# Kernel tuning notes

Measured on AMD Instinct MI355X. Metric: run time of the kernel, lower is better.

## Reference

```python
import jax, jax.numpy as jnp
import numpy as np

B, C, D, O = 64, 64, 512, 256
N_REG, G = 8, 8  # 8 regions of 8 channels


def setup_inputs() -> dict:
    key = jax.random.key(0)
    ks = jax.random.split(key, 9)
    std = 0.02  # init_weights_classify: normal(0, 0.02) for Linear weights, zero bias
    x = jax.random.normal(ks[0], (B, C, D), dtype=jnp.float32)
    region_indices = jnp.arange(C, dtype=jnp.int32).reshape(N_REG, G)
    # attn_fc: Linear(2D -> D), ReLU, Linear(D -> 1)
    W1 = jax.random.normal(ks[1], (2 * D, D), dtype=jnp.float32) * std
    b1 = jnp.zeros((D,), jnp.float32)
    W2 = jax.random.normal(ks[2], (D, 1), dtype=jnp.float32) * std
    b2 = jnp.zeros((1,), jnp.float32)
    # gcn1: Linear(D -> D); gcn2: Linear(D -> O)
    Wg1 = jax.random.normal(ks[3], (D, D), dtype=jnp.float32) * std
    bg1 = jnp.zeros((D,), jnp.float32)
    Wg2 = jax.random.normal(ks[4], (D, O), dtype=jnp.float32) * std
    bg2 = jnp.zeros((O,), jnp.float32)
    return {"x": x, "W1": W1, "b1": b1, "W2": W2, "b2": b2,
            "Wg1": Wg1, "bg1": bg1, "Wg2": Wg2, "bg2": bg2,
            "region_indices": region_indices}


def _leaky_relu02(z):
    return jnp.where(z >= 0, z, 0.2 * z)


def reference(x, W1, b1, W2, b2, Wg1, bg1, Wg2, bg2, region_indices):
    Bb, Cc, Dd = x.shape
    n_reg, g = region_indices.shape
    # channel -> region id; mask[i,j] = same region and i != j
    rid = jnp.zeros((Cc,), jnp.int32).at[region_indices.reshape(-1)].set(
        jnp.repeat(jnp.arange(n_reg, dtype=jnp.int32), g))
    idx = jnp.arange(Cc)
    mask = (rid[:, None] == rid[None, :]) & (idx[:, None] != idx[None, :])  # [C, C]
    # attn_fc on cat(x_i, x_j): split first linear to avoid [B,C,C,2D] concat
    a = x @ W1[:Dd]   # [B, C, D]
    bpart = x @ W1[Dd:]  # [B, C, D]
    h = jax.nn.relu(a[:, :, None, :] + bpart[:, None, :, :] + b1)  # [B, C, C, D]
    scores = jnp.einsum('bijd,do->bij', h, W2) + b2[0]  # [B, C, C]
    scores = jnp.where(mask[None, :, :], scores, -jnp.inf)
    adj = jax.nn.softmax(scores, axis=-1)  # [B, C, C]
    # gcn1: adj @ x -> Linear -> LeakyReLU(0.2); residual mix
    m1 = jnp.einsum('bij,bjd->bid', adj, x)
    x1 = _leaky_relu02(m1 @ Wg1 + bg1)
    x1 = 0.5 * x1 + 0.5 * x
    # gcn2
    m2 = jnp.einsum('bij,bjd->bid', adj, x1)
    out = _leaky_relu02(m2 @ Wg2 + bg2)  # [B, C, O]
    return out
```

## Files before the change

### kernel.cpp

```cpp
#include <hip/hip_runtime.h>
#include <math.h>

#define B_   64
#define C_   64
#define D_   512
#define O_   256
#define G_   8
#define M_   4096

typedef __attribute__((ext_vector_type(8))) short s16x8;
typedef __attribute__((ext_vector_type(4))) float f32x4;
typedef unsigned short u16;
typedef unsigned int   u32;

__device__ __forceinline__ float bf2f(u16 u) { return __uint_as_float(((u32)u) << 16); }
__device__ __forceinline__ u16 f2bf(float f) {
    u32 u = __float_as_uint(f);
    return (u16)((u + 0x7FFFu + ((u >> 16) & 1u)) >> 16);
}
__device__ __forceinline__ void gload16(const void* g, void* l) {
    __builtin_amdgcn_global_load_lds((const __attribute__((address_space(1))) u32*)g,
                                     (__attribute__((address_space(3))) u32*)l, 16, 0, 0);
}
__device__ __forceinline__ void xcd_swz(int& bx, int& by) {
    int nx = (int)gridDim.x;
    int L = bx + by * nx;
    int nwg = nx * (int)gridDim.y;
    int nid = (L & 7) * (nwg >> 3) + (L >> 3);
    bx = nid & (nx - 1);
    by = nid / nx;
}

__global__ __launch_bounds__(256)
void prep_kernel(const float* __restrict__ x, u16* __restrict__ x_bf,
                 const float* __restrict__ W1, u16* __restrict__ W1t,
                 const float* __restrict__ Wg1, u16* __restrict__ Wg1t,
                 const float* __restrict__ Wg2, u16* __restrict__ Wg2t)
{
    __shared__ float tile[32][33];
    const int bx = blockIdx.x, tid = threadIdx.x;
    if (bx < 1024) {
        size_t i = ((size_t)bx * 256 + tid) * 8;
        const float4* p = (const float4*)(x + i);
        float4 v0 = p[0], v1 = p[1];
        s16x8 o;
        o[0] = (short)f2bf(v0.x); o[1] = (short)f2bf(v0.y);
        o[2] = (short)f2bf(v0.z); o[3] = (short)f2bf(v0.w);
        o[4] = (short)f2bf(v1.x); o[5] = (short)f2bf(v1.y);
        o[6] = (short)f2bf(v1.z); o[7] = (short)f2bf(v1.w);
        *(s16x8*)(x_bf + i) = o;
        return;
    }
    const float* src; u16* dst; int k0, n0, nsrc, obase;
    if (bx < 1536) {
        int idx = bx - 1024, h = idx >> 8, t = idx & 255;
        src = W1 + (size_t)h * 512 * 512; dst = W1t; obase = h * 512;
        k0 = (t >> 4) * 32; n0 = (t & 15) * 32; nsrc = 512;
    } else if (bx < 1792) {
        int t = bx - 1536;
        src = Wg1; dst = Wg1t; obase = 0;
        k0 = (t >> 4) * 32; n0 = (t & 15) * 32; nsrc = 512;
    } else {
        int t = bx - 1792;
        src = Wg2; dst = Wg2t; obase = 0;
        k0 = (t >> 3) * 32; n0 = (t & 7) * 32; nsrc = 256;
    }
    int tx = tid & 31, ty = tid >> 5;
    #pragma unroll
    for (int j = 0; j < 4; j++)
        tile[ty + j * 8][tx] = src[(size_t)(k0 + ty + j * 8) * nsrc + n0 + tx];
    __syncthreads();
    #pragma unroll
    for (int j = 0; j < 4; j++)
        dst[(size_t)(obase + n0 + ty + j * 8) * 512 + k0 + tx] = f2bf(tile[tx][ty + j * 8]);
}

__global__ __launch_bounds__(512)
void gemm1_kernel(const u16* __restrict__ A, const u16* __restrict__ Bt,
                  u16* __restrict__ Obf0, u16* __restrict__ Obf1)
{
    constexpr int K = 512, BK = 64, NT = K / BK;
    __shared__ __align__(16) u16 As[2][128 * 64];
    __shared__ __align__(16) u16 Bs[2][128 * 64];

    const int tid = threadIdx.x;
    const int lane = tid & 63;
    const int w = tid >> 6;
    const int wr = w >> 1, wc = w & 1;
    const int lr = lane & 15, lq = lane >> 4;
    int bx = blockIdx.x, by = blockIdx.y;
    xcd_swz(bx, by);
    const int m0 = by * 128, n0 = bx * 128;

    const int sr = tid >> 3;
    const int ss = tid & 7;
    const int gsl = ss ^ (sr & 7);

    f32x4 acc[2][4] = {};

    auto stage = [&](int buf, int kt) {
        #pragma unroll
        for (int ch = 0; ch < 2; ch++)
            gload16(A + (size_t)(m0 + ch * 64 + sr) * K + kt + gsl * 8,
                    &As[buf][ch * 4096 + tid * 8]);
        #pragma unroll
        for (int ch = 0; ch < 2; ch++)
            gload16(Bt + (size_t)(n0 + ch * 64 + sr) * K + kt + gsl * 8,
                    &Bs[buf][ch * 4096 + tid * 8]);
    };

    stage(0, 0);
    int cur = 0;
    for (int t = 0; t < NT; t++) {
        __syncthreads();
        if (t + 1 < NT) stage(cur ^ 1, (t + 1) * BK);
        const u16* as = As[cur]; const u16* bs = Bs[cur];
        #pragma unroll
        for (int ks = 0; ks < 2; ks++) {
            s16x8 af[2], bfv[4];
            #pragma unroll
            for (int m = 0; m < 2; m++) {
                int r = wr * 32 + m * 16 + lr;
                af[m] = *(const s16x8*)(as + r * 64 + (((ks * 4 + lq) ^ (r & 7)) * 8));
            }
            #pragma unroll
            for (int n = 0; n < 4; n++) {
                int r = wc * 64 + n * 16 + lr;
                bfv[n] = *(const s16x8*)(bs + r * 64 + (((ks * 4 + lq) ^ (r & 7)) * 8));
            }
            #pragma unroll
            for (int m = 0; m < 2; m++)
                #pragma unroll
                for (int n = 0; n < 4; n++)
                    acc[m][n] = __builtin_amdgcn_mfma_f32_16x16x32_bf16(af[m], bfv[n], acc[m][n], 0, 0, 0);
        }
        cur ^= 1;
    }

    #pragma unroll
    for (int m = 0; m < 2; m++) {
        #pragma unroll
        for (int n = 0; n < 4; n++) {
            #pragma unroll
            for (int j = 0; j < 4; j++) {
                int row = m0 + wr * 32 + m * 16 + lq * 4 + j;
                int col = n0 + wc * 64 + n * 16 + lr;
                float v = acc[m][n][j];
                if (col < 512) Obf0[(size_t)row * 512 + col] = f2bf(v);
                else           Obf1[(size_t)row * 512 + col - 512] = f2bf(v);
            }
        }
    }
}

__global__ __launch_bounds__(256)
void scores_m1_kernel(const u16* __restrict__ a_bf, const u16* __restrict__ bp_bf,
                      const u16* __restrict__ x_bf,
                      const float* __restrict__ b1, const float* __restrict__ W2,
                      const float* __restrict__ b2,
                      const int* __restrict__ region_indices,
                      float* __restrict__ adjw, u16* __restrict__ m1)
{
    __shared__ __align__(16) u16 bp_lds[64 * 512];
    __shared__ int ri_lds[64];
    __shared__ int rid_lds[64];

    int L = blockIdx.x;
    int nid = ((L & 7) << 5) + (L >> 3);
    const int b = nid >> 2, q = nid & 3;
    const int tid = threadIdx.x, lane = tid & 63, w = tid >> 6;

    #pragma unroll
    for (int it = 0; it < 16; it++)
        gload16(bp_bf + (size_t)b * 32768 + it * 2048 + tid * 8, bp_lds + it * 2048 + tid * 8);
    if (tid < 64) {
        int c = region_indices[tid];
        ri_lds[tid] = c;
        rid_lds[c] = tid >> 3;
    }

    const int d0 = lane * 8;
    float4 b1a = *(const float4*)(b1 + d0), b1b = *(const float4*)(b1 + d0 + 4);
    float4 w2a = *(const float4*)(W2 + d0), w2b = *(const float4*)(W2 + d0 + 4);
    float b1v[8] = { b1a.x, b1a.y, b1a.z, b1a.w, b1b.x, b1b.y, b1b.z, b1b.w };
    float w2v[8] = { w2a.x, w2a.y, w2a.z, w2a.w, w2b.x, w2b.y, w2b.z, w2b.w };
    const float bias2 = b2[0];

    __syncthreads();

    for (int rr = 0; rr < 4; rr++) {
        const int i = q * 16 + w * 4 + rr;
        const int bi = b * 64 + i;
        const int r = rid_lds[i];
        int mem[8];
        #pragma unroll
        for (int m = 0; m < 8; m++) mem[m] = ri_lds[r * 8 + m];

        s16x8 a8 = *(const s16x8*)(a_bf + (size_t)bi * 512 + d0);
        float ai[8];
        #pragma unroll
        for (int t = 0; t < 8; t++) ai[t] = bf2f((u16)a8[t]) + b1v[t];

        float p[8];
        #pragma unroll
        for (int m = 0; m < 8; m++) {
            s16x8 bv = *(const s16x8*)(bp_lds + mem[m] * 512 + d0);
            float s = 0.f;
            #pragma unroll
            for (int t = 0; t < 8; t++) {
                float h = ai[t] + bf2f((u16)bv[t]);
                s += fmaxf(h, 0.f) * w2v[t];
            }
            p[m] = s;
        }
        #pragma unroll
        for (int off = 32; off >= 1; off >>= 1)
            #pragma unroll
            for (int m = 0; m < 8; m++) p[m] += __shfl_xor(p[m], off);

        float scmax = -INFINITY;
        #pragma unroll
        for (int m = 0; m < 8; m++) {
            p[m] = (mem[m] == i) ? -INFINITY : p[m] + bias2;
            scmax = fmaxf(scmax, p[m]);
        }
        float esum = 0.f;
        #pragma unroll
        for (int m = 0; m < 8; m++) {
            p[m] = (mem[m] == i) ? 0.f : __expf(p[m] - scmax);
            esum += p[m];
        }
        const float inv = 1.f / esum;

        float accv[8] = {};
        #pragma unroll
        for (int m = 0; m < 8; m++) {
            p[m] *= inv;
            s16x8 xv = *(const s16x8*)(x_bf + ((size_t)(b * 64 + mem[m])) * 512 + d0);
            #pragma unroll
            for (int t = 0; t < 8; t++) accv[t] += p[m] * bf2f((u16)xv[t]);
        }
        s16x8 o;
        #pragma unroll
        for (int t = 0; t < 8; t++) o[t] = (short)f2bf(accv[t]);
        *(s16x8*)(m1 + (size_t)bi * 512 + d0) = o;
        if (lane < 8) adjw[(size_t)bi * 8 + lane] = p[lane];
    }
}

__global__ __launch_bounds__(512)
void gemm2_m2_kernel(const u16* __restrict__ A, const u16* __restrict__ Bt,
                     const float* __restrict__ bias, const float* __restrict__ xres,
                     const float* __restrict__ adjw, const int* __restrict__ region_indices,
                     u16* __restrict__ m2)
{
    constexpr int K = 512, BK = 64, NT = K / BK;
    __shared__ __align__(16) u16 As[2][64 * 64];
    __shared__ __align__(16) u16 Bs[2][128 * 64];
    __shared__ __align__(16) u16 x1s[64 * 136];
    __shared__ int ri_lds[64];
    __shared__ int rid_lds[64];

    const int tid = threadIdx.x;
    const int lane = tid & 63;
    const int w = tid >> 6;
    const int wr = w >> 2, wc = w & 3;
    const int lr = lane & 15, lq = lane >> 4;
    int bx = blockIdx.x, by = blockIdx.y;
    xcd_swz(bx, by);
    const int b = by, n0 = bx * 128, m0 = b * 64;

    const int sr = tid >> 3, ss = tid & 7;
    const int gsl = ss ^ (sr & 7);

    if (tid < 64) {
        int c = region_indices[tid];
        ri_lds[tid] = c;
        rid_lds[c] = tid >> 3;
    }

    f32x4 acc[2][2] = {};

    auto stage = [&](int buf, int kt) {
        gload16(A + (size_t)(m0 + sr) * K + kt + gsl * 8, &As[buf][tid * 8]);
        #pragma unroll
        for (int ch = 0; ch < 2; ch++)
            gload16(Bt + (size_t)(n0 + ch * 64 + sr) * K + kt + gsl * 8,
                    &Bs[buf][ch * 4096 + tid * 8]);
    };

    stage(0, 0);
    int cur = 0;
    for (int t = 0; t < NT; t++) {
        __syncthreads();
        if (t + 1 < NT) stage(cur ^ 1, (t + 1) * BK);
        const u16* as = As[cur]; const u16* bs = Bs[cur];
        #pragma unroll
        for (int ks = 0; ks < 2; ks++) {
            s16x8 af[2], bfv[2];
            #pragma unroll
            for (int m = 0; m < 2; m++) {
                int r = wr * 32 + m * 16 + lr;
                af[m] = *(const s16x8*)(as + r * 64 + (((ks * 4 + lq) ^ (r & 7)) * 8));
            }
            #pragma unroll
            for (int n = 0; n < 2; n++) {
                int r = wc * 32 + n * 16 + lr;
                bfv[n] = *(const s16x8*)(bs + r * 64 + (((ks * 4 + lq) ^ (r & 7)) * 8));
            }
            #pragma unroll
            for (int m = 0; m < 2; m++)
                #pragma unroll
                for (int n = 0; n < 2; n++)
                    acc[m][n] = __builtin_amdgcn_mfma_f32_16x16x32_bf16(af[m], bfv[n], acc[m][n], 0, 0, 0);
        }
        cur ^= 1;
    }

    #pragma unroll
    for (int m = 0; m < 2; m++) {
        #pragma unroll
        for (int n = 0; n < 2; n++) {
            #pragma unroll
            for (int j = 0; j < 4; j++) {
                int lrow = wr * 32 + m * 16 + lq * 4 + j;
                int lcol = wc * 32 + n * 16 + lr;
                float v = acc[m][n][j] + bias[n0 + lcol];
                v = (v >= 0.f) ? v : 0.2f * v;
                v = 0.5f * v + 0.5f * xres[(size_t)(m0 + lrow) * 512 + n0 + lcol];
                x1s[lrow * 136 + lcol] = f2bf(v);
            }
        }
    }
    __syncthreads();

    const int i = tid >> 3, cb = tid & 7, c0 = cb * 16;
    const int bi = m0 + i;
    const int r = rid_lds[i];
    float acc2[16] = {};
    #pragma unroll
    for (int m = 0; m < 8; m++) {
        float wm = adjw[(size_t)bi * 8 + m];
        int j = ri_lds[r * 8 + m];
        #pragma unroll
        for (int cc = 0; cc < 2; cc++) {
            s16x8 v = *(const s16x8*)(x1s + j * 136 + c0 + cc * 8);
            #pragma unroll
            for (int t = 0; t < 8; t++) acc2[cc * 8 + t] += wm * bf2f((u16)v[t]);
        }
    }
    #pragma unroll
    for (int cc = 0; cc < 2; cc++) {
        s16x8 o;
        #pragma unroll
        for (int t = 0; t < 8; t++) o[t] = (short)f2bf(acc2[cc * 8 + t]);
        *(s16x8*)(m2 + (size_t)bi * 512 + n0 + c0 + cc * 8) = o;
    }
}

__global__ __launch_bounds__(256)
void gemm3_kernel(const u16* __restrict__ A, const u16* __restrict__ Bt,
                  const float* __restrict__ bias, float* __restrict__ Of)
{
    constexpr int K = 512, BK = 64, NT = K / BK;
    __shared__ __align__(16) u16 As[2][64 * 64];
    __shared__ __align__(16) u16 Bs[2][64 * 64];

    const int tid = threadIdx.x;
    const int lane = tid & 63;
    const int w = tid >> 6, wr = w >> 1, wc = w & 1;
    const int lr = lane & 15, lq = lane >> 4;
    int bx = blockIdx.x, by = blockIdx.y;
    xcd_swz(bx, by);
    const int m0 = by * 64, n0 = bx * 64;

    const int sr = tid >> 3, ss = tid & 7;
    const int gsl = ss ^ (sr & 7);

    f32x4 acc[2][2] = {};

    auto stage = [&](int buf, int kt) {
        #pragma unroll
        for (int ch = 0; ch < 2; ch++)
            gload16(A + (size_t)(m0 + ch * 32 + sr) * K + kt + gsl * 8,
                    &As[buf][ch * 2048 + tid * 8]);
        #pragma unroll
        for (int ch = 0; ch < 2; ch++)
            gload16(Bt + (size_t)(n0 + ch * 32 + sr) * K + kt + gsl * 8,
                    &Bs[buf][ch * 2048 + tid * 8]);
    };

    stage(0, 0);
    int cur = 0;
    for (int t = 0; t < NT; t++) {
        __syncthreads();
        if (t + 1 < NT) stage(cur ^ 1, (t + 1) * BK);
        const u16* as = As[cur]; const u16* bs = Bs[cur];
        #pragma unroll
        for (int ks = 0; ks < 2; ks++) {
            s16x8 af[2], bfv[2];
            #pragma unroll
            for (int m = 0; m < 2; m++) {
                int r = wr * 32 + m * 16 + lr;
                af[m] = *(const s16x8*)(as + r * 64 + (((ks * 4 + lq) ^ (r & 7)) * 8));
            }
            #pragma unroll
            for (int n = 0; n < 2; n++) {
                int r = wc * 32 + n * 16 + lr;
                bfv[n] = *(const s16x8*)(bs + r * 64 + (((ks * 4 + lq) ^ (r & 7)) * 8));
            }
            #pragma unroll
            for (int m = 0; m < 2; m++)
                #pragma unroll
                for (int n = 0; n < 2; n++)
                    acc[m][n] = __builtin_amdgcn_mfma_f32_16x16x32_bf16(af[m], bfv[n], acc[m][n], 0, 0, 0);
        }
        cur ^= 1;
    }

    #pragma unroll
    for (int m = 0; m < 2; m++) {
        #pragma unroll
        for (int n = 0; n < 2; n++) {
            #pragma unroll
            for (int j = 0; j < 4; j++) {
                int row = m0 + wr * 32 + m * 16 + lq * 4 + j;
                int col = n0 + wc * 32 + n * 16 + lr;
                float v = acc[m][n][j] + bias[col];
                v = (v >= 0.f) ? v : 0.2f * v;
                Of[(size_t)row * 256 + col] = v;
            }
        }
    }
}

extern "C" void kernel_launch(void* const* d_in, const int* in_sizes, int n_in,
                              void* d_out, int out_size, void* d_ws, size_t ws_size,
                              hipStream_t stream) {
    const float* x    = (const float*)d_in[0];
    const float* W1   = (const float*)d_in[1];
    const float* b1   = (const float*)d_in[2];
    const float* W2   = (const float*)d_in[3];
    const float* b2   = (const float*)d_in[4];
    const float* Wg1  = (const float*)d_in[5];
    const float* bg1  = (const float*)d_in[6];
    const float* Wg2  = (const float*)d_in[7];
    const float* bg2  = (const float*)d_in[8];
    const int* region_indices = (const int*)d_in[9];
    float* out = (float*)d_out;

    char* ws = (char*)d_ws;
    const size_t MB = 1024 * 1024;
    u16*   x_bf  = (u16*)(ws);
    u16*   W1t   = (u16*)(ws + 4 * MB);
    u16*   Wg1t  = (u16*)(ws + 5 * MB);
    u16*   Wg2t  = (u16*)(ws + 5 * MB + 512 * 1024);
    u16*   a_bf  = (u16*)(ws + 6 * MB);
    u16*   bp_bf = (u16*)(ws + 10 * MB);
    u16*   m1_bf = (u16*)(ws + 14 * MB);
    u16*   m2_bf = (u16*)(ws + 18 * MB);
    float* adjw  = (float*)(ws + 22 * MB);

    prep_kernel<<<1920, 256, 0, stream>>>(x, x_bf, W1, W1t, Wg1, Wg1t, Wg2, Wg2t);

    gemm1_kernel<<<dim3(8, 32), 512, 0, stream>>>(x_bf, W1t, a_bf, bp_bf);

    scores_m1_kernel<<<256, 256, 0, stream>>>(a_bf, bp_bf, x_bf, b1, W2, b2,
                                              region_indices, adjw, m1_bf);

    gemm2_m2_kernel<<<dim3(4, 64), 512, 0, stream>>>(
        m1_bf, Wg1t, bg1, x, adjw, region_indices, m2_bf);

    gemm3_kernel<<<dim3(4, 64), 256, 0, stream>>>(m2_bf, Wg2t, bg2, out);
}
```

Before: 119.2 us.

## Fuse five kernels into one persistent kernel with software grid barriers

Replaces the prep, gemm1, scores, gemm2 and gemm3 launches with a single persistent kernel of 256 workgroups of 512 threads, separated by atomic-counter grid barriers. The aim is to remove per-launch overhead and inter-kernel gaps for a small problem. Per-stage work is redistributed to fit the fixed 256-block grid, for example two rows per wave in the scores stage. In exchange it relies on all 256 blocks being co-resident, adds barrier spin cost, and needs a memset before each launch.

```diff
diff --git a/kernel.cpp b/kernel.cpp
--- a/kernel.cpp
+++ b/kernel.cpp
@@ -22,415 +22,361 @@
     __builtin_amdgcn_global_load_lds((const __attribute__((address_space(1))) u32*)g,
                                      (__attribute__((address_space(3))) u32*)l, 16, 0, 0);
 }
-__device__ __forceinline__ void xcd_swz(int& bx, int& by) {
-    int nx = (int)gridDim.x;
-    int L = bx + by * nx;
-    int nwg = nx * (int)gridDim.y;
-    int nid = (L & 7) * (nwg >> 3) + (L >> 3);
-    bx = nid & (nx - 1);
-    by = nid / nx;
+__device__ __forceinline__ int swz256(int L) { return (L & 7) * 32 + (L >> 3); }
+
+__device__ __forceinline__ void grid_barrier(u32* bar, int tid, int nb) {
+    __syncthreads();
+    if (tid == 0) {
+        __threadfence();
+        u32 gen = __hip_atomic_load(bar + 1, __ATOMIC_RELAXED, __HIP_MEMORY_SCOPE_AGENT);
+        u32 arrived = __hip_atomic_fetch_add(bar, 1u, __ATOMIC_ACQ_REL, __HIP_MEMORY_SCOPE_AGENT);
+        if (arrived == (u32)nb - 1) {
+            __hip_atomic_store(bar, 0u, __ATOMIC_RELAXED, __HIP_MEMORY_SCOPE_AGENT);
+            __hip_atomic_fetch_add(bar + 1, 1u, __ATOMIC_RELEASE, __HIP_MEMORY_SCOPE_AGENT);
+        } else {
+            while (__hip_atomic_load(bar + 1, __ATOMIC_ACQUIRE, __HIP_MEMORY_SCOPE_AGENT) == gen)
+                __builtin_amdgcn_s_sleep(8);
+        }
+        __threadfence();
+    }
+    __syncthreads();
 }
 
-__global__ __launch_bounds__(256)
-void prep_kernel(const float* __restrict__ x, u16* __restrict__ x_bf,
-                 const float* __restrict__ W1, u16* __restrict__ W1t,
-                 const float* __restrict__ Wg1, u16* __restrict__ Wg1t,
-                 const float* __restrict__ Wg2, u16* __restrict__ Wg2t)
+#define SMEM_BYTES 69632
+
+__global__ __launch_bounds__(512)
+void fused_kernel(const float* __restrict__ x, const float* __restrict__ W1,
+                  const float* __restrict__ b1, const float* __restrict__ W2,
+                  const float* __restrict__ b2, const float* __restrict__ Wg1,
+                  const float* __restrict__ bg1, const float* __restrict__ Wg2,
+                  const float* __restrict__ bg2, const int* __restrict__ region_indices,
+                  float* __restrict__ out,
+                  u16* __restrict__ x_bf, u16* __restrict__ W1t, u16* __restrict__ Wg1t,
+                  u16* __restrict__ Wg2t, u16* __restrict__ a_bf, u16* __restrict__ bp_bf,
+                  u16* __restrict__ m1_bf, u16* __restrict__ m2_bf,
+                  float* __restrict__ adjw, u32* __restrict__ bar)
 {
-    __shared__ float tile[32][33];
-    const int bx = blockIdx.x, tid = threadIdx.x;
-    if (bx < 1024) {
-        size_t i = ((size_t)bx * 256 + tid) * 8;
-        const float4* p = (const float4*)(x + i);
-        float4 v0 = p[0], v1 = p[1];
-        s16x8 o;
-        o[0] = (short)f2bf(v0.x); o[1] = (short)f2bf(v0.y);
-        o[2] = (short)f2bf(v0.z); o[3] = (short)f2bf(v0.w);
-        o[4] = (short)f2bf(v1.x); o[5] = (short)f2bf(v1.y);
-        o[6] = (short)f2bf(v1.z); o[7] = (short)f2bf(v1.w);
-        *(s16x8*)(x_bf + i) = o;
-        return;
-    }
-    const float* src; u16* dst; int k0, n0, nsrc, obase;
-    if (bx < 1536) {
-        int idx = bx - 1024, h = idx >> 8, t = idx & 255;
-        src = W1 + (size_t)h * 512 * 512; dst = W1t; obase = h * 512;
-        k0 = (t >> 4) * 32; n0 = (t & 15) * 32; nsrc = 512;
-    } else if (bx < 1792) {
-        int t = bx - 1536;
-        src = Wg1; dst = Wg1t; obase = 0;
-        k0 = (t >> 4) * 32; n0 = (t & 15) * 32; nsrc = 512;
-    } else {
-        int t = bx - 1792;
-        src = Wg2; dst = Wg2t; obase = 0;
-        k0 = (t >> 3) * 32; n0 = (t & 7) * 32; nsrc = 256;
-    }
-    int tx = tid & 31, ty = tid >> 5;
-    #pragma unroll
-    for (int j = 0; j < 4; j++)
-        tile[ty + j * 8][tx] = src[(size_t)(k0 + ty + j * 8) * nsrc + n0 + tx];
-    __syncthreads();
-    #pragma unroll
-    for (int j = 0; j < 4; j++)
-        dst[(size_t)(obase + n0 + ty + j * 8) * 512 + k0 + tx] = f2bf(tile[tx][ty + j * 8]);
-}
-
-__global__ __launch_bounds__(512)
-void gemm1_kernel(const u16* __restrict__ A, const u16* __restrict__ Bt,
-                  u16* __restrict__ Obf0, u16* __restrict__ Obf1)
-{
-    constexpr int K = 512, BK = 64, NT = K / BK;
-    __shared__ __align__(16) u16 As[2][128 * 64];
-    __shared__ __align__(16) u16 Bs[2][128 * 64];
-
-    const int tid = threadIdx.x;
-    const int lane = tid & 63;
-    const int w = tid >> 6;
-    const int wr = w >> 1, wc = w & 1;
+    __shared__ __align__(16) char sm[SMEM_BYTES];
+    const int wg = blockIdx.x, tid = threadIdx.x;
+    const int lane = tid & 63, w = tid >> 6;
     const int lr = lane & 15, lq = lane >> 4;
-    int bx = blockIdx.x, by = blockIdx.y;
-    xcd_swz(bx, by);
-    const int m0 = by * 128, n0 = bx * 128;
-
-    const int sr = tid >> 3;
-    const int ss = tid & 7;
-    const int gsl = ss ^ (sr & 7);
-
-    f32x4 acc[2][4] = {};
-
-    auto stage = [&](int buf, int kt) {
-        #pragma unroll
-        for (int ch = 0; ch < 2; ch++)
-            gload16(A + (size_t)(m0 + ch * 64 + sr) * K + kt + gsl * 8,
-                    &As[buf][ch * 4096 + tid * 8]);
-        #pragma unroll
-        for (int ch = 0; ch < 2; ch++)
-            gload16(Bt + (size_t)(n0 + ch * 64 + sr) * K + kt + gsl * 8,
-                    &Bs[buf][ch * 4096 + tid * 8]);
-    };
-
-    stage(0, 0);
-    int cur = 0;
-    for (int t = 0; t < NT; t++) {
+    const int sr = tid >> 3, ss = tid & 7, gsl = ss ^ (sr & 7);
+    const int NB = 256;
+
+    {
+        #pragma unroll
+        for (int s = 0; s < 2; s++) {
+            size_t i = ((size_t)(s * 256 + wg) * 512 + tid) * 8;
+            const float4* p = (const float4*)(x + i);
+            float4 v0 = p[0], v1 = p[1];
+            s16x8 o;
+            o[0]=(short)f2bf(v0.x); o[1]=(short)f2bf(v0.y); o[2]=(short)f2bf(v0.z); o[3]=(short)f2bf(v0.w);
+            o[4]=(short)f2bf(v1.x); o[5]=(short)f2bf(v1.y); o[6]=(short)f2bf(v1.z); o[7]=(short)f2bf(v1.w);
+            *(s16x8*)(x_bf + i) = o;
+        }
+        float (*tile)[32][33] = (float(*)[32][33])sm;
+        const int team = tid >> 8, t = tid & 255;
+        const int tx = t & 31, ty = t >> 5;
+        for (int u = 0; u < 2; u++) {
+            int tile_id = wg * 2 + team + 512 * u;
+            const float* src = nullptr; u16* dst = nullptr;
+            int k0 = 0, n0 = 0, nsrc = 0, obase = 0;
+            if (tile_id < 512) {
+                int h = tile_id >> 8, tt = tile_id & 255;
+                src = W1 + (size_t)h * 512 * 512; dst = W1t; obase = h * 512;
+                k0 = (tt >> 4) * 32; n0 = (tt & 15) * 32; nsrc = 512;
+            } else if (tile_id < 768) {
+                int tt = tile_id - 512; src = Wg1; dst = Wg1t;
+                k0 = (tt >> 4) * 32; n0 = (tt & 15) * 32; nsrc = 512;
+            } else if (tile_id < 896) {
+                int tt = tile_id - 768; src = Wg2; dst = Wg2t;
+                k0 = (tt >> 3) * 32; n0 = (tt & 7) * 32; nsrc = 256;
+            }
+            if (src) {
+                #pragma unroll
+                for (int j = 0; j < 4; j++)
+                    tile[team][ty + j * 8][tx] = src[(size_t)(k0 + ty + j * 8) * nsrc + n0 + tx];
+            }
+            __syncthreads();
+            if (src) {
+                #pragma unroll
+                for (int j = 0; j < 4; j++)
+                    dst[(size_t)(obase + n0 + ty + j * 8) * 512 + k0 + tx] =
+                        f2bf(tile[team][tx][ty + j * 8]);
+            }
+            __syncthreads();
+        }
+    }
+    grid_barrier(bar, tid, NB);
+
+    {
+        u16* As = (u16*)sm;
+        u16* Bs = (u16*)(sm + 32768);
+        const int nid = swz256(wg);
+        const int m0 = (nid >> 3) * 128, n0 = (nid & 7) * 128;
+        const int wr = w >> 1, wc = w & 1;
+        f32x4 acc[2][4] = {};
+        auto stage = [&](int buf, int kt) {
+            #pragma unroll
+            for (int ch = 0; ch < 2; ch++)
+                gload16(x_bf + (size_t)(m0 + ch * 64 + sr) * 512 + kt + gsl * 8,
+                        As + buf * 8192 + ch * 4096 + tid * 8);
+            #pragma unroll
+            for (int ch = 0; ch < 2; ch++)
+                gload16(W1t + (size_t)(n0 + ch * 64 + sr) * 512 + kt + gsl * 8,
+                        Bs + buf * 8192 + ch * 4096 + tid * 8);
+        };
+        stage(0, 0);
+        int cur = 0;
+        for (int t = 0; t < 8; t++) {
+            __syncthreads();
+            if (t < 7) stage(cur ^ 1, (t + 1) * 64);
+            const u16* as = As + cur * 8192;
+            const u16* bs = Bs + cur * 8192;
+            #pragma unroll
+            for (int ks = 0; ks < 2; ks++) {
+                s16x8 af[2], bfv[4];
+                #pragma unroll
+                for (int m = 0; m < 2; m++) {
+                    int r = wr * 32 + m * 16 + lr;
+                    af[m] = *(const s16x8*)(as + r * 64 + (((ks * 4 + lq) ^ (r & 7)) * 8));
+                }
+                #pragma unroll
+                for (int n = 0; n < 4; n++) {
+                    int r = wc * 64 + n * 16 + lr;
+                    bfv[n] = *(const s16x8*)(bs + r * 64 + (((ks * 4 + lq) ^ (r & 7)) * 8));
+                }
+                #pragma unroll
+                for (int m = 0; m < 2; m++)
+                    #pragma unroll
+                    for (int n = 0; n < 4; n++)
+                        acc[m][n] = __builtin_amdgcn_mfma_f32_16x16x32_bf16(af[m], bfv[n], acc[m][n], 0, 0, 0);
+            }
+            cur ^= 1;
+        }
+        #pragma unroll
+        for (int m = 0; m < 2; m++)
+            #pragma unroll
+            for (int n = 0; n < 4; n++)
+                #pragma unroll
+                for (int j = 0; j < 4; j++) {
+                    int row = m0 + wr * 32 + m * 16 + lq * 4 + j;
+                    int col = n0 + wc * 64 + n * 16 + lr;
+                    float v = acc[m][n][j];
+                    if (col < 512) a_bf[(size_t)row * 512 + col] = f2bf(v);
+                    else           bp_bf[(size_t)row * 512 + col - 512] = f2bf(v);
+                }
+    }
+    grid_barrier(bar, tid, NB);
+
+    {
+        u16* bp  = (u16*)sm;
+        int* ri  = (int*)(sm + 65536);
+        int* rid = (int*)(sm + 65536 + 256);
+        const int nid = swz256(wg);
+        const int b = nid >> 2, q = nid & 3;
+        #pragma unroll
+        for (int it = 0; it < 8; it++)
+            gload16(bp_bf + (size_t)b * 32768 + it * 4096 + tid * 8, bp + it * 4096 + tid * 8);
+        if (tid < 64) { int c = region_indices[tid]; ri[tid] = c; rid[c] = tid >> 3; }
+
+        const int d0 = lane * 8;
+        float4 b1a = *(const float4*)(b1 + d0), b1b = *(const float4*)(b1 + d0 + 4);
+        float4 w2a = *(const float4*)(W2 + d0), w2b = *(const float4*)(W2 + d0 + 4);
+        float b1v[8] = { b1a.x, b1a.y, b1a.z, b1a.w, b1b.x, b1b.y, b1b.z, b1b.w };
+        float w2v[8] = { w2a.x, w2a.y, w2a.z, w2a.w, w2b.x, w2b.y, w2b.z, w2b.w };
+        const float bias2 = b2[0];
         __syncthreads();
-        if (t + 1 < NT) stage(cur ^ 1, (t + 1) * BK);
-        const u16* as = As[cur]; const u16* bs = Bs[cur];
-        #pragma unroll
-        for (int ks = 0; ks < 2; ks++) {
-            s16x8 af[2], bfv[4];
-            #pragma unroll
-            for (int m = 0; m < 2; m++) {
-                int r = wr * 32 + m * 16 + lr;
-                af[m] = *(const s16x8*)(as + r * 64 + (((ks * 4 + lq) ^ (r & 7)) * 8));
-            }
-            #pragma unroll
-            for (int n = 0; n < 4; n++) {
-                int r = wc * 64 + n * 16 + lr;
-                bfv[n] = *(const s16x8*)(bs + r * 64 + (((ks * 4 + lq) ^ (r & 7)) * 8));
-            }
-            #pragma unroll
-            for (int m = 0; m < 2; m++)
-                #pragma unroll
-                for (int n = 0; n < 4; n++)
-                    acc[m][n] = __builtin_amdgcn_mfma_f32_16x16x32_bf16(af[m], bfv[n], acc[m][n], 0, 0, 0);
-        }
-        cur ^= 1;
-    }
-
-    #pragma unroll
-    for (int m = 0; m < 2; m++) {
-        #pragma unroll
-        for (int n = 0; n < 4; n++) {
+
+        #pragma unroll
+        for (int rr = 0; rr < 2; rr++) {
+            const int i = q * 16 + w * 2 + rr;
+            const int bi = b * 64 + i;
+            const int r = rid[i];
+            int mem[8];
+            #pragma unroll
+            for (int m = 0; m < 8; m++) mem[m] = ri[r * 8 + m];
+
+            s16x8 a8 = *(const s16x8*)(a_bf + (size_t)bi * 512 + d0);
+            float ai[8];
+            #pragma unroll
+            for (int t = 0; t < 8; t++) ai[t] = bf2f((u16)a8[t]) + b1v[t];
+
+            float p[8];
+            #pragma unroll
+            for (int m = 0; m < 8; m++) {
+                s16x8 bv = *(const s16x8*)(bp + mem[m] * 512 + d0);
+                float s = 0.f;
+                #pragma unroll
+                for (int t = 0; t < 8; t++) {
+                    float h = ai[t] + bf2f((u16)bv[t]);
+                    s += fmaxf(h, 0.f) * w2v[t];
+                }
+                p[m] = s;
+            }
+            #pragma unroll
+            for (int off = 32; off >= 1; off >>= 1)
+                #pragma unroll
+                for (int m = 0; m < 8; m++) p[m] += __shfl_xor(p[m], off);
+
+            float scmax = -INFINITY;
+            #pragma unroll
+            for (int m = 0; m < 8; m++) {
+                p[m] = (mem[m] == i) ? -INFINITY : p[m] + bias2;
+                scmax = fmaxf(scmax, p[m]);
+            }
+            float esum = 0.f;
+            #pragma unroll
+            for (int m = 0; m < 8; m++) {
+                p[m] = (mem[m] == i) ? 0.f : __expf(p[m] - scmax);
+                esum += p[m];
+            }
+            const float inv = 1.f / esum;
+
+            float accv[8] = {};
+            #pragma unroll
+            for (int m = 0; m < 8; m++) {
+                p[m] *= inv;
+                s16x8 xv = *(const s16x8*)(x_bf + ((size_t)(b * 64 + mem[m])) * 512 + d0);
+                #pragma unroll
+                for (int t = 0; t < 8; t++) accv[t] += p[m] * bf2f((u16)xv[t]);
+            }
+            s16x8 o;
+            #pragma unroll
+            for (int t = 0; t < 8; t++) o[t] = (short)f2bf(accv[t]);
+            *(s16x8*)(m1_bf + (size_t)bi * 512 + d0) = o;
+            if (lane < 8) adjw[(size_t)bi * 8 + lane] = p[lane];
+        }
+    }
+    grid_barrier(bar, tid, NB);
+
+    {
+        u16* As  = (u16*)sm;
+        u16* Bs  = (u16*)(sm + 16384);
+        u16* x1s = (u16*)(sm + 49152);
+        int* ri  = (int*)(sm + 66560);
+        int* rid = (int*)(sm + 66816);
+        const int nid = swz256(wg);
+        const int b = nid >> 2, n0 = (nid & 3) * 128, m0 = b * 64;
+        const int wr = w >> 2, wc = w & 3;
+        if (tid < 64) { int c = region_indices[tid]; ri[tid] = c; rid[c] = tid >> 3; }
+
+        f32x4 acc[2][2] = {};
+        auto stage = [&](int buf, int kt) {
+            gload16(m1_bf + (size_t)(m0 + sr) * 512 + kt + gsl * 8, As + buf * 4096 + tid * 8);
+            #pragma unroll
+            for (int ch = 0; ch < 2; ch++)
+                gload16(Wg1t + (size_t)(n0 + ch * 64 + sr) * 512 + kt + gsl * 8,
+                        Bs + buf * 8192 + ch * 4096 + tid * 8);
+        };
+        stage(0, 0);
+        int cur = 0;
+        for (int t = 0; t < 8; t++) {
+            __syncthreads();
+            if (t < 7) stage(cur ^ 1, (t + 1) * 64);
+            const u16* as = As + cur * 4096;
+            const u16* bs = Bs + cur * 8192;
+            #pragma unroll
+            for (int ks = 0; ks < 2; ks++) {
+                s16x8 af[2], bfv[2];
+                #pragma unroll
+                for (int m = 0; m < 2; m++) {
+                    int r = wr * 32 + m * 16 + lr;
+                    af[m] = *(const s16x8*)(as + r * 64 + (((ks * 4 + lq) ^ (r & 7)) * 8));
+                }
+                #pragma unroll
+                for (int n = 0; n < 2; n++) {
+                    int r = wc * 32 + n * 16 + lr;
+                    bfv[n] = *(const s16x8*)(bs + r * 64 + (((ks * 4 + lq) ^ (r & 7)) * 8));
+                }
+                #pragma unroll
+                for (int m = 0; m < 2; m++)
+                    #pragma unroll
+                    for (int n = 0; n < 2; n++)
+                        acc[m][n] = __builtin_amdgcn_mfma_f32_16x16x32_bf16(af[m], bfv[n], acc[m][n], 0, 0, 0);
+            }
+            cur ^= 1;
+        }
+        #pragma unroll
+        for (int m = 0; m < 2; m++)
+            #pragma unroll
+            for (int n = 0; n < 2; n++)
+                #pragma unroll
+                for (int j = 0; j < 4; j++) {
+                    int lrow = wr * 32 + m * 16 + lq * 4 + j;
+                    int lcol = wc * 32 + n * 16 + lr;
+                    float v = acc[m][n][j] + bg1[n0 + lcol];
+                    v = (v >= 0.f) ? v : 0.2f * v;
+                    v = 0.5f * v + 0.5f * x[(size_t)(m0 + lrow) * 512 + n0 + lcol];
+                    x1s[lrow * 136 + lcol] = f2bf(v);
+                }
+        __syncthreads();
+        const int i = tid >> 3, cb = tid & 7, c0 = cb * 16;
+        const int bi = m0 + i;
+        const int r = rid[i];
+        float acc2[16] = {};
+        #pragma unroll
+        for (int m = 0; m < 8; m++) {
+            float wm = adjw[(size_t)bi * 8 + m];
+            int j = ri[r * 8 + m];
+            #pragma unroll
+            for (int cc = 0; cc < 2; cc++) {
+                s16x8 v = *(const s16x8*)(x1s + j * 136 + c0 + cc * 8);
+                #pragma unroll
+                for (int t = 0; t < 8; t++) acc2[cc * 8 + t] += wm * bf2f((u16)v[t]);
+            }
+        }
+        #pragma unroll
+        for (int cc = 0; cc < 2; cc++) {
+            s16x8 o;
+            #pragma unroll
+            for (int t = 0; t < 8; t++) o[t] = (short)f2bf(acc2[cc * 8 + t]);
+            *(s16x8*)(m2_bf + (size_t)bi * 512 + n0 + c0 + cc * 8) = o;
+        }
+    }
+    grid_barrier(bar, tid, NB);
+
+    {
+        u16* As = (u16*)sm;
+        u16* Bs = (u16*)(sm + 16384);
+        const int nid = swz256(wg);
+        const int m0 = (nid >> 2) * 64, n0 = (nid & 3) * 64;
+        const int wr = w >> 1, wc = w & 1;
+        f32x4 acc[2] = {};
+        auto stage = [&](int buf, int kt) {
+            gload16(m2_bf + (size_t)(m0 + sr) * 512 + kt + gsl * 8, As + buf * 4096 + tid * 8);
+            gload16(Wg2t + (size_t)(n0 + sr) * 512 + kt + gsl * 8, Bs + buf * 4096 + tid * 8);
+        };
+        stage(0, 0);
+        int cur = 0;
+        for (int t = 0; t < 8; t++) {
+            __syncthreads();
+            if (t < 7) stage(cur ^ 1, (t + 1) * 64);
+            const u16* as = As + cur * 4096;
+            const u16* bs = Bs + cur * 4096;
+            #pragma unroll
+            for (int ks = 0; ks < 2; ks++) {
+                int ra = wr * 16 + lr;
+                s16x8 af = *(const s16x8*)(as + ra * 64 + (((ks * 4 + lq) ^ (ra & 7)) * 8));
+                #pragma unroll
+                for (int n = 0; n < 2; n++) {
+                    int r = wc * 32 + n * 16 + lr;
+                    s16x8 bv = *(const s16x8*)(bs + r * 64 + (((ks * 4 + lq) ^ (r & 7)) * 8));
+                    acc[n] = __builtin_amdgcn_mfma_f32_16x16x32_bf16(af, bv, acc[n], 0, 0, 0);
+                }
+            }
+            cur ^= 1;
+        }
+        #pragma unroll
+        for (int n = 0; n < 2; n++)
             #pragma unroll
             for (int j = 0; j < 4; j++) {
-                int row = m0 + wr * 32 + m * 16 + lq * 4 + j;
-                int col = n0 + wc * 64 + n * 16 + lr;
-                float v = acc[m][n][j];
-                if (col < 512) Obf0[(size_t)row * 512 + col] = f2bf(v);
-                else           Obf1[(size_t)row * 512 + col - 512] = f2bf(v);
-            }
-        }
-    }
-}
-
-__global__ __launch_bounds__(256)
-void scores_m1_kernel(const u16* __restrict__ a_bf, const u16* __restrict__ bp_bf,
-                      const u16* __restrict__ x_bf,
-                      const float* __restrict__ b1, const float* __restrict__ W2,
-                      const float* __restrict__ b2,
-                      const int* __restrict__ region_indices,
-                      float* __restrict__ adjw, u16* __restrict__ m1)
-{
-    __shared__ __align__(16) u16 bp_lds[64 * 512];
-    __shared__ int ri_lds[64];
-    __shared__ int rid_lds[64];
-
-    int L = blockIdx.x;
-    int nid = ((L & 7) << 5) + (L >> 3);
-    const int b = nid >> 2, q = nid & 3;
-    const int tid = threadIdx.x, lane = tid & 63, w = tid >> 6;
-
-    #pragma unroll
-    for (int it = 0; it < 16; it++)
-        gload16(bp_bf + (size_t)b * 32768 + it * 2048 + tid * 8, bp_lds + it * 2048 + tid * 8);
-    if (tid < 64) {
-        int c = region_indices[tid];
-        ri_lds[tid] = c;
-        rid_lds[c] = tid >> 3;
-    }
-
-    const int d0 = lane * 8;
-    float4 b1a = *(const float4*)(b1 + d0), b1b = *(const float4*)(b1 + d0 + 4);
-    float4 w2a = *(const float4*)(W2 + d0), w2b = *(const float4*)(W2 + d0 + 4);
-    float b1v[8] = { b1a.x, b1a.y, b1a.z, b1a.w, b1b.x, b1b.y, b1b.z, b1b.w };
-    float w2v[8] = { w2a.x, w2a.y, w2a.z, w2a.w, w2b.x, w2b.y, w2b.z, w2b.w };
-    const float bias2 = b2[0];
-
-    __syncthreads();
-
-    for (int rr = 0; rr < 4; rr++) {
-        const int i = q * 16 + w * 4 + rr;
-        const int bi = b * 64 + i;
-        const int r = rid_lds[i];
-        int mem[8];
-        #pragma unroll
-        for (int m = 0; m < 8; m++) mem[m] = ri_lds[r * 8 + m];
-
-        s16x8 a8 = *(const s16x8*)(a_bf + (size_t)bi * 512 + d0);
-        float ai[8];
-        #pragma unroll
-        for (int t = 0; t < 8; t++) ai[t] = bf2f((u16)a8[t]) + b1v[t];
-
-        float p[8];
-        #pragma unroll
-        for (int m = 0; m < 8; m++) {
-            s16x8 bv = *(const s16x8*)(bp_lds + mem[m] * 512 + d0);
-            float s = 0.f;
-            #pragma unroll
-            for (int t = 0; t < 8; t++) {
-                float h = ai[t] + bf2f((u16)bv[t]);
-                s += fmaxf(h, 0.f) * w2v[t];
-            }
-            p[m] = s;
-        }
-        #pragma unroll
-        for (int off = 32; off >= 1; off >>= 1)
-            #pragma unroll
-            for (int m = 0; m < 8; m++) p[m] += __shfl_xor(p[m], off);
-
-        float scmax = -INFINITY;
-        #pragma unroll
-        for (int m = 0; m < 8; m++) {
-            p[m] = (mem[m] == i) ? -INFINITY : p[m] + bias2;
-            scmax = fmaxf(scmax, p[m]);
-        }
-        float esum = 0.f;
-        #pragma unroll
-        for (int m = 0; m < 8; m++) {
-            p[m] = (mem[m] == i) ? 0.f : __expf(p[m] - scmax);
-            esum += p[m];
-        }
-        const float inv = 1.f / esum;
-
-        float accv[8] = {};
-        #pragma unroll
-        for (int m = 0; m < 8; m++) {
-            p[m] *= inv;
-            s16x8 xv = *(const s16x8*)(x_bf + ((size_t)(b * 64 + mem[m])) * 512 + d0);
-            #pragma unroll
-            for (int t = 0; t < 8; t++) accv[t] += p[m] * bf2f((u16)xv[t]);
-        }
-        s16x8 o;
-        #pragma unroll
-        for (int t = 0; t < 8; t++) o[t] = (short)f2bf(accv[t]);
-        *(s16x8*)(m1 + (size_t)bi * 512 + d0) = o;
-        if (lane < 8) adjw[(size_t)bi * 8 + lane] = p[lane];
-    }
-}
-
-__global__ __launch_bounds__(512)
-void gemm2_m2_kernel(const u16* __restrict__ A, const u16* __restrict__ Bt,
-                     const float* __restrict__ bias, const float* __restrict__ xres,
-                     const float* __restrict__ adjw, const int* __restrict__ region_indices,
-                     u16* __restrict__ m2)
-{
-    constexpr int K = 512, BK = 64, NT = K / BK;
-    __shared__ __align__(16) u16 As[2][64 * 64];
-    __shared__ __align__(16) u16 Bs[2][128 * 64];
-    __shared__ __align__(16) u16 x1s[64 * 136];
-    __shared__ int ri_lds[64];
-    __shared__ int rid_lds[64];
-
-    const int tid = threadIdx.x;
-    const int lane = tid & 63;
-    const int w = tid >> 6;
-    const int wr = w >> 2, wc = w & 3;
-    const int lr = lane & 15, lq = lane >> 4;
-    int bx = blockIdx.x, by = blockIdx.y;
-    xcd_swz(bx, by);
-    const int b = by, n0 = bx * 128, m0 = b * 64;
-
-    const int sr = tid >> 3, ss = tid & 7;
-    const int gsl = ss ^ (sr & 7);
-
-    if (tid < 64) {
-        int c = region_indices[tid];
-        ri_lds[tid] = c;
-        rid_lds[c] = tid >> 3;
-    }
-
-    f32x4 acc[2][2] = {};
-
-    auto stage = [&](int buf, int kt) {
-        gload16(A + (size_t)(m0 + sr) * K + kt + gsl * 8, &As[buf][tid * 8]);
-        #pragma unroll
-        for (int ch = 0; ch < 2; ch++)
-            gload16(Bt + (size_t)(n0 + ch * 64 + sr) * K + kt + gsl * 8,
-                    &Bs[buf][ch * 4096 + tid * 8]);
-    };
-
-    stage(0, 0);
-    int cur = 0;
-    for (int t = 0; t < NT; t++) {
-        __syncthreads();
-        if (t + 1 < NT) stage(cur ^ 1, (t + 1) * BK);
-        const u16* as = As[cur]; const u16* bs = Bs[cur];
-        #pragma unroll
-        for (int ks = 0; ks < 2; ks++) {
-            s16x8 af[2], bfv[2];
-            #pragma unroll
-            for (int m = 0; m < 2; m++) {
-                int r = wr * 32 + m * 16 + lr;
-                af[m] = *(const s16x8*)(as + r * 64 + (((ks * 4 + lq) ^ (r & 7)) * 8));
-            }
-            #pragma unroll
-            for (int n = 0; n < 2; n++) {
-                int r = wc * 32 + n * 16 + lr;
-                bfv[n] = *(const s16x8*)(bs + r * 64 + (((ks * 4 + lq) ^ (r & 7)) * 8));
-            }
-            #pragma unroll
-            for (int m = 0; m < 2; m++)
-                #pragma unroll
-                for (int n = 0; n < 2; n++)
-                    acc[m][n] = __builtin_amdgcn_mfma_f32_16x16x32_bf16(af[m], bfv[n], acc[m][n], 0, 0, 0);
-        }
-        cur ^= 1;
-    }
-
-    #pragma unroll
-    for (int m = 0; m < 2; m++) {
-        #pragma unroll
-        for (int n = 0; n < 2; n++) {
-            #pragma unroll
-            for (int j = 0; j < 4; j++) {
-                int lrow = wr * 32 + m * 16 + lq * 4 + j;
-                int lcol = wc * 32 + n * 16 + lr;
-                float v = acc[m][n][j] + bias[n0 + lcol];
+                int row = m0 + wr * 16 + lq * 4 + j;
+                int col = n0 + wc * 32 + n * 16 + lr;
+                float v = acc[n][j] + bg2[col];
                 v = (v >= 0.f) ? v : 0.2f * v;
-                v = 0.5f * v + 0.5f * xres[(size_t)(m0 + lrow) * 512 + n0 + lcol];
-                x1s[lrow * 136 + lcol] = f2bf(v);
-            }
-        }
-    }
-    __syncthreads();
-
-    const int i = tid >> 3, cb = tid & 7, c0 = cb * 16;
-    const int bi = m0 + i;
-    const int r = rid_lds[i];
-    float acc2[16] = {};
-    #pragma unroll
-    for (int m = 0; m < 8; m++) {
-        float wm = adjw[(size_t)bi * 8 + m];
-        int j = ri_lds[r * 8 + m];
-        #pragma unroll
-        for (int cc = 0; cc < 2; cc++) {
-            s16x8 v = *(const s16x8*)(x1s + j * 136 + c0 + cc * 8);
-            #pragma unroll
-            for (int t = 0; t < 8; t++) acc2[cc * 8 + t] += wm * bf2f((u16)v[t]);
-        }
-    }
-    #pragma unroll
-    for (int cc = 0; cc < 2; cc++) {
-        s16x8 o;
-        #pragma unroll
-        for (int t = 0; t < 8; t++) o[t] = (short)f2bf(acc2[cc * 8 + t]);
-        *(s16x8*)(m2 + (size_t)bi * 512 + n0 + c0 + cc * 8) = o;
-    }
-}
-
-__global__ __launch_bounds__(256)
-void gemm3_kernel(const u16* __restrict__ A, const u16* __restrict__ Bt,
-                  const float* __restrict__ bias, float* __restrict__ Of)
-{
-    constexpr int K = 512, BK = 64, NT = K / BK;
-    __shared__ __align__(16) u16 As[2][64 * 64];
-    __shared__ __align__(16) u16 Bs[2][64 * 64];
-
-    const int tid = threadIdx.x;
-    const int lane = tid & 63;
-    const int w = tid >> 6, wr = w >> 1, wc = w & 1;
-    const int lr = lane & 15, lq = lane >> 4;
-    int bx = blockIdx.x, by = blockIdx.y;
-    xcd_swz(bx, by);
-    const int m0 = by * 64, n0 = bx * 64;
-
-    const int sr = tid >> 3, ss = tid & 7;
-    const int gsl = ss ^ (sr & 7);
-
-    f32x4 acc[2][2] = {};
-
-    auto stage = [&](int buf, int kt) {
-        #pragma unroll
-        for (int ch = 0; ch < 2; ch++)
-            gload16(A + (size_t)(m0 + ch * 32 + sr) * K + kt + gsl * 8,
-                    &As[buf][ch * 2048 + tid * 8]);
-        #pragma unroll
-        for (int ch = 0; ch < 2; ch++)
-            gload16(Bt + (size_t)(n0 + ch * 32 + sr) * K + kt + gsl * 8,
-                    &Bs[buf][ch * 2048 + tid * 8]);
-    };
-
-    stage(0, 0);
-    int cur = 0;
-    for (int t = 0; t < NT; t++) {
-        __syncthreads();
-        if (t + 1 < NT) stage(cur ^ 1, (t + 1) * BK);
-        const u16* as = As[cur]; const u16* bs = Bs[cur];
-        #pragma unroll
-        for (int ks = 0; ks < 2; ks++) {
-            s16x8 af[2], bfv[2];
-            #pragma unroll
-            for (int m = 0; m < 2; m++) {
-                int r = wr * 32 + m * 16 + lr;
-                af[m] = *(const s16x8*)(as + r * 64 + (((ks * 4 + lq) ^ (r & 7)) * 8));
-            }
-            #pragma unroll
-            for (int n = 0; n < 2; n++) {
-                int r = wc * 32 + n * 16 + lr;
-                bfv[n] = *(const s16x8*)(bs + r * 64 + (((ks * 4 + lq) ^ (r & 7)) * 8));
-            }
-            #pragma unroll
-            for (int m = 0; m < 2; m++)
-                #pragma unroll
-                for (int n = 0; n < 2; n++)
-                    acc[m][n] = __builtin_amdgcn_mfma_f32_16x16x32_bf16(af[m], bfv[n], acc[m][n], 0, 0, 0);
-        }
-        cur ^= 1;
-    }
-
-    #pragma unroll
-    for (int m = 0; m < 2; m++) {
-        #pragma unroll
-        for (int n = 0; n < 2; n++) {
-            #pragma unroll
-            for (int j = 0; j < 4; j++) {
-                int row = m0 + wr * 32 + m * 16 + lq * 4 + j;
-                int col = n0 + wc * 32 + n * 16 + lr;
-                float v = acc[m][n][j] + bias[col];
-                v = (v >= 0.f) ? v : 0.2f * v;
-                Of[(size_t)row * 256 + col] = v;
-            }
-        }
+                out[(size_t)row * 256 + col] = v;
+            }
     }
 }
 
@@ -460,16 +406,11 @@
     u16*   m1_bf = (u16*)(ws + 14 * MB);
     u16*   m2_bf = (u16*)(ws + 18 * MB);
     float* adjw  = (float*)(ws + 22 * MB);
-
-    prep_kernel<<<1920, 256, 0, stream>>>(x, x_bf, W1, W1t, Wg1, Wg1t, Wg2, Wg2t);
-
-    gemm1_kernel<<<dim3(8, 32), 512, 0, stream>>>(x_bf, W1t, a_bf, bp_bf);
-
-    scores_m1_kernel<<<256, 256, 0, stream>>>(a_bf, bp_bf, x_bf, b1, W2, b2,
-                                              region_indices, adjw, m1_bf);
-
-    gemm2_m2_kernel<<<dim3(4, 64), 512, 0, stream>>>(
-        m1_bf, Wg1t, bg1, x, adjw, region_indices, m2_bf);
-
-    gemm3_kernel<<<dim3(4, 64), 256, 0, stream>>>(m2_bf, Wg2t, bg2, out);
+    u32*   bar   = (u32*)(ws + 32 * MB);
+
+    hipMemsetAsync(bar, 0, 64, stream);
+
+    fused_kernel<<<256, 512, 0, stream>>>(
+        x, W1, b1, W2, b2, Wg1, bg1, Wg2, bg2, region_indices, out,
+        x_bf, W1t, Wg1t, Wg2t, a_bf, bp_bf, m1_bf, m2_bf, adjw, bar);
 }
```

Result: slower. 261.4 us (+119.2%).
